# Performance work log

Measured on AMD Instinct MI355X. Metric: run time of the kernel, lower is better.

Reference implementation:

```python
import jax, jax.numpy as jnp
import numpy as np

N_HOPS = 2
NEG_SLOPE = 0.2


def setup_inputs() -> dict:
    key = jax.random.key(0)
    k1, k2, k3, k4, k5 = jax.random.split(key, 5)
    N, E, D, R = 100000, 1600000, 64, 64
    edge_index = jax.random.randint(k1, (2, E), 0, N, dtype=jnp.int64)
    edge_type = jax.random.randint(k2, (E,), 0, R, dtype=jnp.int64)
    entity_emb = jax.random.normal(k3, (N, D), dtype=jnp.float32) * 0.1
    relation_emb = jax.random.normal(k4, (R, D), dtype=jnp.float32) * 0.1
    W = jax.random.normal(k5, (2 * D, D), dtype=jnp.float32) * 0.1
    return {"edge_index": edge_index, "edge_type": edge_type,
            "entity_emb": entity_emb, "relation_emb": relation_emb, "W": W}


def _hop(emb, head, tail, rel_e, W, N):
    # gather head/tail embeddings: [E, 2D]
    a_input = jnp.concatenate([emb[head], emb[tail]], axis=-1)
    # relation-gated attention logit per edge: [E]
    e = jnp.sum((a_input @ W) * rel_e, axis=-1)
    e = jax.nn.leaky_relu(e, NEG_SLOPE)
    # scatter-softmax grouped by head node
    seg_max = jax.ops.segment_max(e, head, num_segments=N)  # [N]
    ex = jnp.exp(e - seg_max[head])
    denom = jax.ops.segment_sum(ex, head, num_segments=N)   # [N]
    alpha = ex / denom[head]
    # weighted scatter-sum aggregation + residual
    agg = jax.ops.segment_sum(emb[tail] * alpha[:, None], head, num_segments=N)
    return agg + emb


def reference(edge_index, edge_type, entity_emb, relation_emb, W):
    head, tail = edge_index[0], edge_index[1]
    N = entity_emb.shape[0]
    rel_e = relation_emb[edge_type]  # [E, D], constant across hops
    res = entity_emb
    emb = entity_emb
    for _ in range(N_HOPS):
        emb = _hop(emb, head, tail, rel_e, W, N)
        # F.normalize: row-wise L2 with eps 1e-12 (dropout disabled)
        norm = jnp.maximum(jnp.linalg.norm(emb, axis=-1, keepdims=True), 1e-12)
        emb = emb / norm
        res = 0.5 * res + emb
    return res
```

## Files before the change

kernel.cpp:

```cpp
#include <hip/hip_runtime.h>


#define NEG_SLOPE 0.2f
#define CAP 64
#define BKT_SHIFT 7
#define SCAP 24
#define NBA 512
#define EPB_MAX 3136

__device__ __forceinline__ float b2f_lo(unsigned x) {
    return __uint_as_float(x << 16);
}
__device__ __forceinline__ float b2f_hi(unsigned x) {
    return __uint_as_float(x & 0xffff0000u);
}
__device__ __forceinline__ unsigned short f2b(float x) {
    unsigned u = __float_as_uint(x);
    unsigned r = u + 0x7fffu + ((u >> 16) & 1u);
    return (unsigned short)(r >> 16);
}

__device__ __forceinline__ float dot2bf(unsigned a, unsigned b, float c) {
    float d;
    asm("v_dot2_f32_bf16 %0, %1, %2, %3" : "=v"(d) : "v"(a), "v"(b), "v"(c));
    return d;
}

__device__ __forceinline__ float ror_sum16(float x) {
#define ROR_ADD(ctrl)                                                          \
    x += __int_as_float(                                                       \
        __builtin_amdgcn_update_dpp(0, __float_as_int(x), ctrl, 0xf, 0xf, true))
    ROR_ADD(0x121);
    ROR_ADD(0x122);
    ROR_ADD(0x124);
    ROR_ADD(0x128);
#undef ROR_ADD
    return x;
}

__global__ __launch_bounds__(512) void buildA_kernel(
    const int* __restrict__ head, const int* __restrict__ tail,
    const int* __restrict__ etype, unsigned* __restrict__ stream,
    unsigned char* __restrict__ cnts, int E4, int nbkt) {
    __shared__ int hist[1024];
    __shared__ int excl[1024];
    __shared__ int tsum[512];
    __shared__ uint2 sortedLDS[EPB_MAX];
    int bid = blockIdx.x;
    int t = threadIdx.x;
    int i0 = (int)((long)bid * E4 / NBA);
    int i1 = (int)((long)(bid + 1) * E4 / NBA);
    int n = (i1 - i0) * 4;
    for (int i = t; i < 1024; i += 512) hist[i] = 0;
    __syncthreads();
    for (int i = i0 + t; i < i1; i += 512) {
        int4 h = *(const int4*)(head + (long)i * 4);
        atomicAdd(&hist[h.x >> BKT_SHIFT], 1);
        atomicAdd(&hist[h.y >> BKT_SHIFT], 1);
        atomicAdd(&hist[h.z >> BKT_SHIFT], 1);
        atomicAdd(&hist[h.w >> BKT_SHIFT], 1);
    }
    __syncthreads();
    int c0 = hist[2 * t], c1 = hist[2 * t + 1];
    int s = c0 + c1;
    tsum[t] = s;
    __syncthreads();
    for (int off = 1; off < 512; off <<= 1) {
        int v = (t >= off) ? tsum[t - off] : 0;
        __syncthreads();
        tsum[t] += v;
        __syncthreads();
    }
    int run = tsum[t] - s;
    hist[2 * t] = run;       excl[2 * t] = run;
    hist[2 * t + 1] = run + c0; excl[2 * t + 1] = run + c0;
    __syncthreads();
    for (int i = i0 + t; i < i1; i += 512) {
        int4 h = *(const int4*)(head + (long)i * 4);
        int4 tl = *(const int4*)(tail + (long)i * 4);
        int4 q = *(const int4*)(etype + (long)i * 4);
#pragma unroll
        for (int u = 0; u < 4; ++u) {
            int hh = (u == 0) ? h.x : (u == 1) ? h.y : (u == 2) ? h.z : h.w;
            int tt = (u == 0) ? tl.x : (u == 1) ? tl.y : (u == 2) ? tl.z : tl.w;
            int qq = (u == 0) ? q.x : (u == 1) ? q.y : (u == 2) ? q.z : q.w;
            int b = hh >> BKT_SHIFT;
            int pos = atomicAdd(&hist[b], 1);
            int local = pos - excl[b];
            unsigned entry = ((unsigned)(hh & 127) << 23) |
                             ((unsigned)tt << 6) | (unsigned)qq;
            unsigned dst = (local < SCAP)
                ? (unsigned)(((long)bid * nbkt + b) * SCAP + local)
                : 0xFFFFFFFFu;
            sortedLDS[pos] = make_uint2(entry, dst);
        }
    }
    __syncthreads();
    for (int i = t; i < n; i += 512) {
        uint2 v = sortedLDS[i];
        if (v.y != 0xFFFFFFFFu) stream[v.y] = v.x;
    }
    for (int b = t; b < nbkt; b += 512)
        cnts[bid * nbkt + b] = (unsigned char)min(hist[b] - excl[b], SCAP);
}

__global__ __launch_bounds__(256) void binB_kernel(
    const unsigned char* __restrict__ cnts, const unsigned* __restrict__ stream,
    int* __restrict__ deg, int* __restrict__ csr, int* __restrict__ perm,
    const float* __restrict__ W, const float* __restrict__ rel,
    unsigned short* __restrict__ Wuvb, const float* __restrict__ ent,
    unsigned short* __restrict__ entb, int nbkt, int N, int n4, int R,
    int wuvB) {
    __shared__ int cnt[128];
    __shared__ int hist[CAP + 2];
    __shared__ unsigned csrS[128 * 65];
    int bid = blockIdx.x;
    int t = threadIdx.x;
    if (bid >= nbkt + wuvB) {
        int i = (bid - nbkt - wuvB) * 1024 + t;
#pragma unroll
        for (int j = 0; j < 4; ++j, i += 256) {
            if (i < n4) {
                float4 v = *(const float4*)(ent + (long)i * 4);
                ushort4 o = {f2b(v.x), f2b(v.y), f2b(v.z), f2b(v.w)};
                *(ushort4*)(entb + (long)i * 4) = o;
            }
        }
        return;
    }
    if (bid >= nbkt) {
        int r = (bid - nbkt) * 2 + (t >> 7);
        int i = t & 127;
        if (r < R) {
            float s = 0.f;
#pragma unroll
            for (int j = 0; j < 64; ++j) s += W[i * 64 + j] * rel[r * 64 + j];
            int d = i & 63, half = i >> 6;
            Wuvb[r * 128 + (d >> 2) * 8 + half * 4 + (d & 3)] = f2b(s);
        }
        return;
    }
    int b = bid;
    if (t < 128) cnt[t] = 0;
    if (t < CAP + 2) hist[t] = 0;
    __syncthreads();
    {
        int lane = t & 7;
        for (int seg = t >> 3; seg < NBA; seg += 32) {
            int c = cnts[seg * nbkt + b];
            const unsigned* sp = stream + ((long)seg * nbkt + b) * SCAP;
            for (int k = lane; k < c; k += 8) {
                unsigned e = sp[k];
                int l = (int)(e >> 23) & 127;
                int p = atomicAdd(&cnt[l], 1);
                if (p < CAP) csrS[l * 65 + p] = e & 0x7FFFFFu;
            }
        }
    }
    __syncthreads();
    int l = t, d = 0, rank = 0;
    bool v = false;
    if (l < 128) {
        int node = (b << BKT_SHIFT) + l;
        v = node < N;
        if (v) {
            deg[node] = cnt[l];
            d = min(cnt[l], CAP);
            rank = atomicAdd(&hist[d], 1);
        }
    }
    __syncthreads();
    if (t == 0) {
        int s = 0;
        for (int i = 0; i <= CAP; ++i) { int tt = hist[i]; hist[i] = s; s += tt; }
    }
    __syncthreads();
    if (v) perm[(b << BKT_SHIFT) + hist[d] + rank] = (b << BKT_SHIFT) + l;
    int w4 = t >> 6, lane = t & 63;
    int q = lane >> 4, sL = lane & 15;
    for (int j = 0; j < 8; ++j) {
        int ln = ((j & 3) << 5) + (q << 3) + ((j >> 2) << 2) + w4;
        int node = (b << BKT_SHIFT) + ln;
        if (node < N) {
            int dcl = min(cnt[ln], CAP);
            for (int r = 0; r * 16 < dcl; ++r)
                csr[(long)node * CAP + r * 16 + sL] =
                    (int)csrS[ln * 65 + r * 16 + sL];
        }
    }
}

__global__ __launch_bounds__(512) void hop_kernel(
    const int* __restrict__ degp, const int* __restrict__ csr,
    const int* __restrict__ perm,
    const unsigned short* __restrict__ Wuvb,
    const unsigned short* __restrict__ embb, const float* res_prev,
    unsigned short* embb_out, float* res_out, int N) {
    __shared__ unsigned short sUV[64 * 136];
    for (int k = threadIdx.x; k < 64 * 128; k += 512) {
        int r = k >> 7, q = k & 127;
        sUV[r * 136 + q] = Wuvb[k];
    }
    __syncthreads();

    int tid = threadIdx.x;
    int s = tid & 15;
    int gi = blockIdx.x * 32 + (tid >> 4);
    bool valid = gi < N;
    int node = valid ? perm[gi] : 0;
    long nb64 = (long)node * 64;

    uint2 hdp = valid ? *(const uint2*)(embb + nb64 + s * 4)
                      : make_uint2(0u, 0u);

    int deg = valid ? min(degp[node], CAP) : 0;
    int r0 = node * CAP;
    int dmin = min(min(__shfl(deg, 0), __shfl(deg, 16)),
                   min(__shfl(deg, 32), __shfl(deg, 48)));
    int dmax = max(max(__shfl(deg, 0), __shfl(deg, 16)),
                   max(__shfl(deg, 32), __shfl(deg, 48)));

    float a0 = 0.f, a1 = 0.f, a2 = 0.f, a3 = 0.f, l = 0.f;

    auto edge_body = [&](int pe, uint2 rw, bool gated, int idx) {
        int rr = pe & 63;
        uint4 uv = *(const uint4*)(sUV + rr * 136 + s * 8);
        float sd = dot2bf(hdp.x, uv.x, 0.f);
        sd = dot2bf(hdp.y, uv.y, sd);
        sd = dot2bf(rw.x, uv.z, sd);
        sd = dot2bf(rw.y, uv.w, sd);
        sd = ror_sum16(sd);
        float p = fmaxf(sd, NEG_SLOPE * sd);
        float w = __expf(p);
        if (gated) w = (idx < deg) ? w : 0.f;
        l += w;
        float e0 = b2f_lo(rw.x), e1 = b2f_hi(rw.x);
        float e2 = b2f_lo(rw.y), e3 = b2f_hi(rw.y);
        a0 += w * e0; a1 += w * e1; a2 += w * e2; a3 += w * e3;
    };

    int c = 0;
    for (; c + 8 <= dmin; c += 8) {
        uint4 ea = *(const uint4*)(csr + r0 + c);
        uint4 eb = *(const uint4*)(csr + r0 + c + 4);
        int pe[8] = {(int)ea.x, (int)ea.y, (int)ea.z, (int)ea.w,
                     (int)eb.x, (int)eb.y, (int)eb.z, (int)eb.w};
        uint2 rw[8];
#pragma unroll
        for (int u = 0; u < 8; ++u)
            rw[u] = *(const uint2*)(embb + (long)(pe[u] >> 6) * 64 + s * 4);
#pragma unroll
        for (int u = 0; u < 8; ++u) edge_body(pe[u], rw[u], false, 0);
    }
    for (; c + 4 <= dmin; c += 4) {
        uint4 e4 = *(const uint4*)(csr + r0 + c);
        int pe[4] = {(int)e4.x, (int)e4.y, (int)e4.z, (int)e4.w};
        uint2 rw[4];
#pragma unroll
        for (int u = 0; u < 4; ++u)
            rw[u] = *(const uint2*)(embb + (long)(pe[u] >> 6) * 64 + s * 4);
#pragma unroll
        for (int u = 0; u < 4; ++u) edge_body(pe[u], rw[u], false, 0);
    }
    for (; c < dmax; c += 4) {
        uint4 e4 = *(const uint4*)(csr + r0 + c);
        int pe[4];
        pe[0] = (c + 0 < deg) ? (int)e4.x : 0;
        pe[1] = (c + 1 < deg) ? (int)e4.y : 0;
        pe[2] = (c + 2 < deg) ? (int)e4.z : 0;
        pe[3] = (c + 3 < deg) ? (int)e4.w : 0;
        uint2 rw[4];
#pragma unroll
        for (int u = 0; u < 4; ++u)
            rw[u] = *(const uint2*)(embb + (long)(pe[u] >> 6) * 64 + s * 4);
#pragma unroll
        for (int u = 0; u < 4; ++u) edge_body(pe[u], rw[u], true, c + u);
    }

    if (valid) {
        float hd0 = b2f_lo(hdp.x), hd1 = b2f_hi(hdp.x);
        float hd2 = b2f_lo(hdp.y), hd3 = b2f_hi(hdp.y);
        float inv = (l > 0.f) ? 1.f / l : 0.f;
        float v0 = hd0 + a0 * inv, v1 = hd1 + a1 * inv;
        float v2 = hd2 + a2 * inv, v3 = hd3 + a3 * inv;
        float sq = v0 * v0 + v1 * v1 + v2 * v2 + v3 * v3;
        sq = ror_sum16(sq);
        float rn = 1.f / fmaxf(sqrtf(sq), 1e-12f);
        v0 *= rn; v1 *= rn; v2 *= rn; v3 *= rn;
        if (embb_out) {
            ushort4 o = {f2b(v0), f2b(v1), f2b(v2), f2b(v3)};
            *(ushort4*)(embb_out + nb64 + s * 4) = o;
        }
        float4 rp = *(const float4*)(res_prev + nb64 + s * 4);
        float4 ro = {0.5f * rp.x + v0, 0.5f * rp.y + v1,
                     0.5f * rp.z + v2, 0.5f * rp.w + v3};
        *(float4*)(res_out + nb64 + s * 4) = ro;
    }
}

extern "C" void kernel_launch(void* const* d_in, const int* in_sizes, int n_in,
                              void* d_out, int out_size, void* d_ws, size_t ws_size,
                              hipStream_t stream_) {
    const int*   edge_index = (const int*)d_in[0];
    const int*   etype      = (const int*)d_in[1];
    const float* ent        = (const float*)d_in[2];
    const float* rel        = (const float*)d_in[3];
    const float* W          = (const float*)d_in[4];

    const int E = in_sizes[1];
    const int N = in_sizes[2] / 64;
    const int R = in_sizes[3] / 64;
    const int* head = edge_index;
    const int* tail = edge_index + E;
    float* out = (float*)d_out;

    const int nbkt = ((N - 1) >> BKT_SHIFT) + 1;

    char* w = (char*)d_ws;
    unsigned short* Wuvb = (unsigned short*)w;  w += (size_t)R * 128 * 2;
    int* deg = (int*)w;                         w += ((size_t)N + 64) * 4;
    int* csr = (int*)w;                         w += (size_t)N * CAP * 4;
    unsigned* bstream = (unsigned*)w;           w += (size_t)NBA * nbkt * SCAP * 4;
    unsigned char* cnts = (unsigned char*)w;    w += ((size_t)NBA * nbkt + 3) & ~3ull;
    unsigned short* entb = (unsigned short*)w;  w += (size_t)N * 64 * 2;
    int* perm = (int*)w;                        w += ((size_t)N + 64) * 4;
    unsigned short* emb1b = (unsigned short*)bstream;

    const int n4 = N * 16;
    const int E4 = E / 4;
    const int wuvB = (R + 1) / 2;
    const int castB = (n4 + 1023) / 1024;
    const int hb = (N + 31) / 32;

    buildA_kernel<<<NBA, 512, 0, stream_>>>(head, tail, etype, bstream,
                                            cnts, E4, nbkt);

    binB_kernel<<<nbkt + wuvB + castB, 256, 0, stream_>>>(
        cnts, bstream, deg, csr, perm, W, rel, Wuvb, ent, entb,
        nbkt, N, n4, R, wuvB);

    hop_kernel<<<hb, 512, 0, stream_>>>(deg, csr, perm, Wuvb, entb, ent,
                                        emb1b, out, N);
    hop_kernel<<<hb, 512, 0, stream_>>>(deg, csr, perm, Wuvb, emb1b, out,
                                        nullptr, out, N);
}
```

Before: 218.3 us.

## Move Wuv and entity bf16 cast into buildA, widen binB to 512 threads

Moves the Wuv precompute and the entity-to-bf16 cast blocks out of the bucket-binning kernel and into the edge-bucketing kernel as extra blocks, so they run alongside the bucketing work. The binning kernel now launches 512 threads per bucket block, halving the per-thread segment loop and reworking the CSR write-out mapping for 32 groups of 16 lanes. This shortens the binB critical path, but buildA blocks use large LDS allocations even for the simple cast blocks, which may limit occupancy for those tail blocks.

```diff
diff --git a/kernel.cpp b/kernel.cpp
--- a/kernel.cpp
+++ b/kernel.cpp
@@ -41,13 +41,37 @@
 __global__ __launch_bounds__(512) void buildA_kernel(
     const int* __restrict__ head, const int* __restrict__ tail,
     const int* __restrict__ etype, unsigned* __restrict__ stream,
-    unsigned char* __restrict__ cnts, int E4, int nbkt) {
+    unsigned char* __restrict__ cnts, const float* __restrict__ W,
+    const float* __restrict__ rel, unsigned short* __restrict__ Wuvb,
+    const float* __restrict__ ent, unsigned short* __restrict__ entb,
+    int E4, int nbkt, int n4, int R) {
     __shared__ int hist[1024];
     __shared__ int excl[1024];
     __shared__ int tsum[512];
     __shared__ uint2 sortedLDS[EPB_MAX];
     int bid = blockIdx.x;
     int t = threadIdx.x;
+    if (bid >= NBA + 16) {
+        int i = (bid - NBA - 16) * 512 + t;
+        if (i < n4) {
+            float4 v = *(const float4*)(ent + (long)i * 4);
+            ushort4 o = {f2b(v.x), f2b(v.y), f2b(v.z), f2b(v.w)};
+            *(ushort4*)(entb + (long)i * 4) = o;
+        }
+        return;
+    }
+    if (bid >= NBA) {
+        int r = (bid - NBA) * 4 + (t >> 7);
+        int i = t & 127;
+        if (r < R) {
+            float s = 0.f;
+#pragma unroll
+            for (int j = 0; j < 64; ++j) s += W[i * 64 + j] * rel[r * 64 + j];
+            int d = i & 63, half = i >> 6;
+            Wuvb[r * 128 + (d >> 2) * 8 + half * 4 + (d & 3)] = f2b(s);
+        }
+        return;
+    }
     int i0 = (int)((long)bid * E4 / NBA);
     int i1 = (int)((long)(bid + 1) * E4 / NBA);
     int n = (i1 - i0) * 4;
@@ -104,49 +128,21 @@
         cnts[bid * nbkt + b] = (unsigned char)min(hist[b] - excl[b], SCAP);
 }
 
-__global__ __launch_bounds__(256) void binB_kernel(
+__global__ __launch_bounds__(512) void binB_kernel(
     const unsigned char* __restrict__ cnts, const unsigned* __restrict__ stream,
     int* __restrict__ deg, int* __restrict__ csr, int* __restrict__ perm,
-    const float* __restrict__ W, const float* __restrict__ rel,
-    unsigned short* __restrict__ Wuvb, const float* __restrict__ ent,
-    unsigned short* __restrict__ entb, int nbkt, int N, int n4, int R,
-    int wuvB) {
+    int nbkt, int N) {
     __shared__ int cnt[128];
     __shared__ int hist[CAP + 2];
     __shared__ unsigned csrS[128 * 65];
-    int bid = blockIdx.x;
+    int b = blockIdx.x;
     int t = threadIdx.x;
-    if (bid >= nbkt + wuvB) {
-        int i = (bid - nbkt - wuvB) * 1024 + t;
-#pragma unroll
-        for (int j = 0; j < 4; ++j, i += 256) {
-            if (i < n4) {
-                float4 v = *(const float4*)(ent + (long)i * 4);
-                ushort4 o = {f2b(v.x), f2b(v.y), f2b(v.z), f2b(v.w)};
-                *(ushort4*)(entb + (long)i * 4) = o;
-            }
-        }
-        return;
-    }
-    if (bid >= nbkt) {
-        int r = (bid - nbkt) * 2 + (t >> 7);
-        int i = t & 127;
-        if (r < R) {
-            float s = 0.f;
-#pragma unroll
-            for (int j = 0; j < 64; ++j) s += W[i * 64 + j] * rel[r * 64 + j];
-            int d = i & 63, half = i >> 6;
-            Wuvb[r * 128 + (d >> 2) * 8 + half * 4 + (d & 3)] = f2b(s);
-        }
-        return;
-    }
-    int b = bid;
     if (t < 128) cnt[t] = 0;
     if (t < CAP + 2) hist[t] = 0;
     __syncthreads();
     {
         int lane = t & 7;
-        for (int seg = t >> 3; seg < NBA; seg += 32) {
+        for (int seg = t >> 3; seg < NBA; seg += 64) {
             int c = cnts[seg * nbkt + b];
             const unsigned* sp = stream + ((long)seg * nbkt + b) * SCAP;
             for (int k = lane; k < c; k += 8) {
@@ -176,16 +172,17 @@
     }
     __syncthreads();
     if (v) perm[(b << BKT_SHIFT) + hist[d] + rank] = (b << BKT_SHIFT) + l;
-    int w4 = t >> 6, lane = t & 63;
-    int q = lane >> 4, sL = lane & 15;
-    for (int j = 0; j < 8; ++j) {
-        int ln = ((j & 3) << 5) + (q << 3) + ((j >> 2) << 2) + w4;
-        int node = (b << BKT_SHIFT) + ln;
-        if (node < N) {
-            int dcl = min(cnt[ln], CAP);
-            for (int r = 0; r * 16 < dcl; ++r)
-                csr[(long)node * CAP + r * 16 + sL] =
-                    (int)csrS[ln * 65 + r * 16 + sL];
+    {
+        int gid = t >> 4, sL = t & 15;
+        for (int j = 0; j < 4; ++j) {
+            int ln = (j << 5) + gid;
+            int node = (b << BKT_SHIFT) + ln;
+            if (node < N) {
+                int dcl = min(cnt[ln], CAP);
+                for (int r = 0; r * 16 < dcl; ++r)
+                    csr[(long)node * CAP + r * 16 + sL] =
+                        (int)csrS[ln * 65 + r * 16 + sL];
+            }
         }
     }
 }
@@ -328,16 +325,15 @@
 
     const int n4 = N * 16;
     const int E4 = E / 4;
-    const int wuvB = (R + 1) / 2;
-    const int castB = (n4 + 1023) / 1024;
+    const int castB = (n4 + 511) / 512;
     const int hb = (N + 31) / 32;
 
-    buildA_kernel<<<NBA, 512, 0, stream_>>>(head, tail, etype, bstream,
-                                            cnts, E4, nbkt);
-
-    binB_kernel<<<nbkt + wuvB + castB, 256, 0, stream_>>>(
-        cnts, bstream, deg, csr, perm, W, rel, Wuvb, ent, entb,
-        nbkt, N, n4, R, wuvB);
+    buildA_kernel<<<NBA + 16 + castB, 512, 0, stream_>>>(
+        head, tail, etype, bstream, cnts, W, rel, Wuvb, ent, entb,
+        E4, nbkt, n4, R);
+
+    binB_kernel<<<nbkt, 512, 0, stream_>>>(cnts, bstream, deg, csr, perm,
+                                           nbkt, N);
 
     hop_kernel<<<hb, 512, 0, stream_>>>(deg, csr, perm, Wuvb, entb, ent,
                                         emb1b, out, N);
```

Measured after the change: 215.1 us. About the same (-1.5%).
